# Kernel optimization log

Hardware: AMD Instinct MI355X
Metric: run time of the kernel (lower is better)

Reference implementation:

```python
import jax, jax.numpy as jnp
import numpy as np

N = 100000          # nodes
E = 3200000         # edges
C_IN = 64
HIDDEN = 64
NUM_CLASSES = 10
NUM_GRAPHS = 256
EPS = 1e-5


def _graph_conv(x, src, dst, w_rel, w_root, b):
    # PyG GraphConv(aggr='mean'): out_i = W_rel * mean_{j->i} x_j + W_root * x_i + b
    msg_sum = jax.ops.segment_sum(x[src], dst, num_segments=N)            # [N, C]
    cnt = jax.ops.segment_sum(jnp.ones((src.shape[0], 1), x.dtype), dst,
                              num_segments=N)                             # [N, 1]
    agg = msg_sum / jnp.maximum(cnt, 1.0)
    return agg @ w_rel + x @ w_root + b


def _batch_norm(x, gamma, beta):
    # PyG BatchNorm in training mode: batch stats over the node dimension
    mean = jnp.mean(x, axis=0)
    var = jnp.var(x, axis=0)
    return (x - mean) * jax.lax.rsqrt(var + EPS) * gamma + beta


def setup_inputs() -> dict:
    key = jax.random.key(0)
    ks = jax.random.split(key, 20)
    x = jax.random.normal(ks[0], (N, C_IN), dtype=jnp.float32)
    edge_index = jax.random.randint(ks[1], (2, E), 0, N, dtype=jnp.int32)
    batch = jnp.sort(jax.random.randint(ks[2], (N,), 0, NUM_GRAPHS, dtype=jnp.int32))

    def lin(k, fan_in, fan_out):
        s = 1.0 / np.sqrt(fan_in)
        return jax.random.uniform(k, (fan_in, fan_out), jnp.float32, -s, s)

    dims = [(C_IN, 16), (16, 32), (32, 32), (32, HIDDEN)]
    params = {}
    ki = 3
    for i, (ci, co) in enumerate(dims, start=1):
        params[f"w_rel{i}"] = lin(ks[ki], ci, co); ki += 1
        params[f"w_root{i}"] = lin(ks[ki], ci, co); ki += 1
        params[f"b{i}"] = jnp.zeros((co,), jnp.float32)
        params[f"g{i}"] = jnp.ones((co,), jnp.float32)
        params[f"be{i}"] = jnp.zeros((co,), jnp.float32)
    params["w_lin1"] = lin(ks[ki], HIDDEN, HIDDEN); ki += 1
    params["b_lin1"] = jnp.zeros((HIDDEN,), jnp.float32)
    params["w_lin2"] = lin(ks[ki], HIDDEN, NUM_CLASSES); ki += 1
    params["b_lin2"] = jnp.zeros((NUM_CLASSES,), jnp.float32)

    return {"x": x, "edge_index": edge_index, "batch": batch, **params}


def reference(x, edge_index, batch,
              w_rel1, w_root1, b1, g1, be1,
              w_rel2, w_root2, b2, g2, be2,
              w_rel3, w_root3, b3, g3, be3,
              w_rel4, w_root4, b4, g4, be4,
              w_lin1, b_lin1, w_lin2, b_lin2):
    src, dst = edge_index[0], edge_index[1]
    h = jax.nn.elu(_batch_norm(_graph_conv(x, src, dst, w_rel1, w_root1, b1), g1, be1))
    h = jax.nn.elu(_batch_norm(_graph_conv(h, src, dst, w_rel2, w_root2, b2), g2, be2))
    h = jax.nn.elu(_batch_norm(_graph_conv(h, src, dst, w_rel3, w_root3, b3), g3, be3))
    h = jax.nn.elu(_batch_norm(_graph_conv(h, src, dst, w_rel4, w_root4, b4), g4, be4))
    # global mean pool over graphs
    pooled = jax.ops.segment_sum(h, batch, num_segments=NUM_GRAPHS)
    cnt = jax.ops.segment_sum(jnp.ones((N, 1), h.dtype), batch, num_segments=NUM_GRAPHS)
    pooled = pooled / jnp.maximum(cnt, 1.0)
    z = jax.nn.relu(pooled @ w_lin1 + b_lin1)
    # dropout omitted (deterministic / eval mode)
    logits = z @ w_lin2 + b_lin2
    return jax.nn.log_softmax(logits, axis=-1)
```

## Files before the change

kernel.cpp:

```cpp
#include <hip/hip_runtime.h>
#include <hip/hip_bf16.h>
#include <math.h>

#define NGRAPHS 256
#define BSHIFT 8
#define NBUCK 512
#define NSORT 256
#define LSTAT 1024
#define GCHUNK 1024
#define SMASK 0x00FFFFFFu

__device__ __forceinline__ float bf2f(unsigned short u) {
    return __uint_as_float((unsigned)u << 16);
}
__device__ __forceinline__ unsigned short f2bf(float f) {
    unsigned u = __float_as_uint(f);
    unsigned r = (u + 0x7FFFu + ((u >> 16) & 1u)) >> 16;
    return (unsigned short)r;
}

__global__ __launch_bounds__(256) void k_bhist(const int* __restrict__ dst, int* __restrict__ hmat, int E,
                                               const float* __restrict__ x, const float* __restrict__ w_rel1,
                                               unsigned short* __restrict__ y1b,
                                               float* __restrict__ zbase, int zwords, int N) {
    int bid = blockIdx.x, tid = threadIdx.x;
    if (bid < NSORT) {
        __shared__ int hist[NBUCK];
        for (int i = tid; i < NBUCK; i += 256) hist[i] = 0;
        __syncthreads();
        int chunk = (E + NSORT - 1) / NSORT;
        int lo = bid * chunk;
        int hi = lo + chunk; if (hi > E) hi = E;
        for (int i = lo + tid; i < hi; i += 256)
            atomicAdd(&hist[__builtin_nontemporal_load(dst + i) >> BSHIFT], 1);
        __syncthreads();
        for (int i = tid; i < NBUCK; i += 256)
            hmat[(size_t)bid * NBUCK + i] = hist[i];
    } else {
        if (bid == NSORT) {
            for (int i = tid; i < zwords; i += 256) zbase[i] = 0.f;
        }
        __shared__ float s_rel[64 * 16];
        for (int i = tid; i < 64 * 16; i += 256) s_rel[i] = w_rel1[i];
        __syncthreads();
        int total = N * 4;
        int nb = gridDim.x - NSORT;
        for (int i = (bid - NSORT) * 256 + tid; i < total; i += nb * 256) {
            int n = i >> 2, c0 = (i & 3) << 2;
            const float4* mp = (const float4*)(x + (size_t)n * 64);
            float4 acc; acc.x = 0.f; acc.y = 0.f; acc.z = 0.f; acc.w = 0.f;
#pragma unroll
            for (int k2 = 0; k2 < 16; k2++) {
                float4 v = mp[k2];
                const float* wr = &s_rel[(k2 * 4) * 16 + c0];
                float4 w0 = *(const float4*)(wr);
                float4 w1 = *(const float4*)(wr + 16);
                float4 w2 = *(const float4*)(wr + 32);
                float4 w3 = *(const float4*)(wr + 48);
                acc.x += v.x * w0.x + v.y * w1.x + v.z * w2.x + v.w * w3.x;
                acc.y += v.x * w0.y + v.y * w1.y + v.z * w2.y + v.w * w3.y;
                acc.z += v.x * w0.z + v.y * w1.z + v.z * w2.z + v.w * w3.z;
                acc.w += v.x * w0.w + v.y * w1.w + v.z * w2.w + v.w * w3.w;
            }
            ushort4 o; o.x = f2bf(acc.x); o.y = f2bf(acc.y); o.z = f2bf(acc.z); o.w = f2bf(acc.w);
            *(ushort4*)(y1b + (size_t)n * 16 + c0) = o;
        }
    }
}

__global__ __launch_bounds__(512) void k_scan(int* __restrict__ hmat, int* __restrict__ bstart) {
    __shared__ int s[512];
    int col = threadIdx.x;
    int run = 0;
#pragma unroll 4
    for (int r = 0; r < NSORT; r++) {
        int v = hmat[(size_t)r * NBUCK + col];
        hmat[(size_t)r * NBUCK + col] = run;
        run += v;
    }
    s[col] = run;
    __syncthreads();
    for (int off = 1; off < 512; off <<= 1) {
        int t = (col >= off) ? s[col - off] : 0;
        __syncthreads();
        s[col] += t;
        __syncthreads();
    }
    bstart[col] = s[col] - run;
    if (col == 511) bstart[NBUCK] = s[511];
}

__global__ __launch_bounds__(256) void k_bscatter(const int* __restrict__ src, const int* __restrict__ dst,
                                                  const int* __restrict__ hmat, const int* __restrict__ bstart,
                                                  unsigned* __restrict__ ebuf, int E) {
    __shared__ int cur[NBUCK];
    for (int i = threadIdx.x; i < NBUCK; i += 256)
        cur[i] = bstart[i] + hmat[(size_t)blockIdx.x * NBUCK + i];
    __syncthreads();
    int chunk = (E + NSORT - 1) / NSORT;
    int lo = blockIdx.x * chunk;
    int hi = lo + chunk; if (hi > E) hi = E;
    for (int i = lo + threadIdx.x; i < hi; i += 256) {
        int d = __builtin_nontemporal_load(dst + i);
        int s = __builtin_nontemporal_load(src + i);
        int p = atomicAdd(&cur[d >> BSHIFT], 1);
        ebuf[p] = (unsigned)s | ((unsigned)(d & 255) << 24);
    }
}

__global__ __launch_bounds__(256) void k_sort2(const unsigned* __restrict__ ebuf, const int* __restrict__ bstart,
                                               int* __restrict__ csr, int* __restrict__ row_start, int N) {
    __shared__ int hist[256];
    __shared__ int sc[256];
    __shared__ int scur[256];
    int b = blockIdx.x;
    int e0 = bstart[b], e1 = bstart[b + 1];
    hist[threadIdx.x] = 0;
    __syncthreads();
    for (int i = e0 + threadIdx.x; i < e1; i += 256)
        atomicAdd(&hist[__builtin_nontemporal_load(ebuf + i) >> 24], 1);
    __syncthreads();
    sc[threadIdx.x] = hist[threadIdx.x];
    __syncthreads();
    for (int off = 1; off < 256; off <<= 1) {
        int t = (threadIdx.x >= off) ? sc[threadIdx.x - off] : 0;
        __syncthreads();
        sc[threadIdx.x] += t;
        __syncthreads();
    }
    {
        int inc = sc[threadIdx.x];
        int ex = inc - hist[threadIdx.x];
        scur[threadIdx.x] = e0 + ex;
        int node = (b << BSHIFT) + threadIdx.x;
        if (node < N) row_start[node] = e0 + ex;
        if (node == N - 1) row_start[N] = e0 + inc;
    }
    __syncthreads();
    for (int i = e0 + threadIdx.x; i < e1; i += 256) {
        unsigned w = __builtin_nontemporal_load(ebuf + i);
        int p = atomicAdd(&scur[w >> 24], 1);
        csr[p] = (int)(w & SMASK);
    }
}

template <int C>
__global__ __launch_bounds__(256) void k_gather(const unsigned short* __restrict__ h,
                                                const int* __restrict__ row_start,
                                                const int* __restrict__ csr, float* __restrict__ agg, int N) {
    constexpr int LPR = C / 4;
    constexpr int EPP = 64 / LPR;
    constexpr int BATCH = 4 * EPP;
    __shared__ int sbuf[GCHUNK];
    int lane = threadIdx.x & 63;
    int w = threadIdx.x >> 6;
    int nb = blockIdx.x * 4;
    int wid = nb + w;
    bool act = wid < N;
    int nb_end = nb + 4; if (nb_end > N) nb_end = N;
    int eb0 = row_start[nb];
    int eb1 = row_start[nb_end];
    int r0 = act ? row_start[wid] : 0;
    int r1 = act ? row_start[wid + 1] : 0;
    int es = lane / LPR;
    int cq = (lane % LPR) * 4;

    float a0 = 0.f, a1 = 0.f, a2 = 0.f, a3 = 0.f;
    for (int base = eb0; base < eb1; base += GCHUNK) {
        int len = eb1 - base; if (len > GCHUNK) len = GCHUNK;
        __syncthreads();
        for (int i = threadIdx.x; i < len; i += 256)
            sbuf[i] = __builtin_nontemporal_load(csr + base + i);
        __syncthreads();
        if (act) {
            int lo = (r0 > base ? r0 : base) - base;
            int hiv = r1 < base + len ? r1 : base + len;
            int hi = hiv - base;
            for (int j0 = lo; j0 < hi; j0 += BATCH) {
                int s[4]; bool p[4];
#pragma unroll
                for (int u = 0; u < 4; u++) {
                    int j = j0 + u * EPP + es;
                    p[u] = j < hi;
                    s[u] = sbuf[p[u] ? j : j0];
                }
                ushort4 v[4];
#pragma unroll
                for (int u = 0; u < 4; u++)
                    v[u] = *(const ushort4*)(h + (size_t)s[u] * C + cq);
#pragma unroll
                for (int u = 0; u < 4; u++) {
                    if (p[u]) {
                        a0 += bf2f(v[u].x); a1 += bf2f(v[u].y);
                        a2 += bf2f(v[u].z); a3 += bf2f(v[u].w);
                    }
                }
            }
        }
    }
#pragma unroll
    for (int off = LPR; off < 64; off <<= 1) {
        a0 += __shfl_xor(a0, off, 64);
        a1 += __shfl_xor(a1, off, 64);
        a2 += __shfl_xor(a2, off, 64);
        a3 += __shfl_xor(a3, off, 64);
    }
    if (act && lane < LPR) {
        int deg = r1 - r0;
        float rec = 1.0f / (float)(deg > 0 ? deg : 1);
        float4 o; o.x = a0 * rec; o.y = a1 * rec; o.z = a2 * rec; o.w = a3 * rec;
        *(float4*)(agg + (size_t)wid * C + cq) = o;
    }
}

template <int CI, int CO, bool HAS_REL, bool ADD_AGG, bool IN_BF16>
__global__ __launch_bounds__(256) void k_lin_stats(const void* __restrict__ hroot_v, const float* __restrict__ hrel,
                                                   const float* __restrict__ w_rel, const float* __restrict__ w_root,
                                                   const float* __restrict__ bias,
                                                   float* __restrict__ out, float* __restrict__ gsl, int N) {
    constexpr int QPR = CO / 4;
    __shared__ float s_rel[HAS_REL ? CI * CO : 1];
    __shared__ float s_root[CI * CO];
    __shared__ float s_b[CO];
    __shared__ float part[4][2 * CO];
    int tid = threadIdx.x;
    if (HAS_REL)
        for (int i = tid; i < CI * CO; i += 256) s_rel[i] = w_rel[i];
    for (int i = tid; i < CI * CO; i += 256) s_root[i] = w_root[i];
    if (tid < CO) s_b[tid] = bias[tid];
    __syncthreads();

    int total = N * QPR;
    int stride = gridDim.x * 256;
    float s0 = 0, s1 = 0, s2 = 0, s3 = 0, q0 = 0, q1 = 0, q2 = 0, q3 = 0;
    for (int i = blockIdx.x * 256 + tid; i < total; i += stride) {
        int n = i / QPR, c0 = (i % QPR) * 4;
        float4 acc = *(const float4*)&s_b[c0];
        if (ADD_AGG) {
            float4 v = ((const float4*)hrel)[i];
            acc.x += v.x; acc.y += v.y; acc.z += v.z; acc.w += v.w;
        }
#pragma unroll
        for (int cb = 0; cb < CI / 4; cb++) {
            float f0, f1, f2, f3;
            if (IN_BF16) {
                ushort4 v = *(const ushort4*)((const unsigned short*)hroot_v + (size_t)n * CI + cb * 4);
                f0 = bf2f(v.x); f1 = bf2f(v.y); f2 = bf2f(v.z); f3 = bf2f(v.w);
            } else {
                float4 v = *(const float4*)((const float*)hroot_v + (size_t)n * CI + cb * 4);
                f0 = v.x; f1 = v.y; f2 = v.z; f3 = v.w;
            }
            const float* wr = &s_root[(cb * 4) * CO + c0];
            float4 w0 = *(const float4*)(wr);
            float4 w1 = *(const float4*)(wr + CO);
            float4 w2 = *(const float4*)(wr + 2 * CO);
            float4 w3 = *(const float4*)(wr + 3 * CO);
            acc.x += f0 * w0.x + f1 * w1.x + f2 * w2.x + f3 * w3.x;
            acc.y += f0 * w0.y + f1 * w1.y + f2 * w2.y + f3 * w3.y;
            acc.z += f0 * w0.z + f1 * w1.z + f2 * w2.z + f3 * w3.z;
            acc.w += f0 * w0.w + f1 * w1.w + f2 * w2.w + f3 * w3.w;
            if (HAS_REL) {
                float4 a = *(const float4*)(hrel + (size_t)n * CI + cb * 4);
                const float* we = &s_rel[(cb * 4) * CO + c0];
                float4 e0 = *(const float4*)(we);
                float4 e1 = *(const float4*)(we + CO);
                float4 e2 = *(const float4*)(we + 2 * CO);
                float4 e3 = *(const float4*)(we + 3 * CO);
                acc.x += a.x * e0.x + a.y * e1.x + a.z * e2.x + a.w * e3.x;
                acc.y += a.x * e0.y + a.y * e1.y + a.z * e2.y + a.w * e3.y;
                acc.z += a.x * e0.z + a.y * e1.z + a.z * e2.z + a.w * e3.z;
                acc.w += a.x * e0.w + a.y * e1.w + a.z * e2.w + a.w * e3.w;
            }
        }
        ((float4*)out)[i] = acc;
        s0 += acc.x; q0 += acc.x * acc.x;
        s1 += acc.y; q1 += acc.y * acc.y;
        s2 += acc.z; q2 += acc.z * acc.z;
        s3 += acc.w; q3 += acc.w * acc.w;
    }
#pragma unroll
    for (int off = QPR; off < 64; off <<= 1) {
        s0 += __shfl_xor(s0, off, 64); q0 += __shfl_xor(q0, off, 64);
        s1 += __shfl_xor(s1, off, 64); q1 += __shfl_xor(q1, off, 64);
        s2 += __shfl_xor(s2, off, 64); q2 += __shfl_xor(q2, off, 64);
        s3 += __shfl_xor(s3, off, 64); q3 += __shfl_xor(q3, off, 64);
    }
    int lane = tid & 63;
    int w = tid >> 6;
    if (lane < QPR) {
        int cq = lane * 4;
        part[w][cq + 0] = s0; part[w][CO + cq + 0] = q0;
        part[w][cq + 1] = s1; part[w][CO + cq + 1] = q1;
        part[w][cq + 2] = s2; part[w][CO + cq + 2] = q2;
        part[w][cq + 3] = s3; part[w][CO + cq + 3] = q3;
    }
    __syncthreads();
    if (tid < 2 * CO) {
        float v = part[0][tid] + part[1][tid] + part[2][tid] + part[3][tid];
        atomicAdd(&gsl[tid], v);
    }
}

template <int CO>
__global__ __launch_bounds__(256) void k_bn_elu(const float* __restrict__ h, const float* __restrict__ gsl,
                                                const float* __restrict__ g, const float* __restrict__ be,
                                                unsigned short* __restrict__ hb, float invN, int N) {
    __shared__ float sc[CO], sh[CO];
    if (threadIdx.x < CO) {
        int c = threadIdx.x;
        float mean = gsl[c] * invN;
        float var = gsl[CO + c] * invN - mean * mean;
        float s = g[c] * rsqrtf(var + 1e-5f);
        sc[c] = s;
        sh[c] = be[c] - mean * s;
    }
    __syncthreads();
    int total = N * (CO / 4);
    int i = blockIdx.x * 256 + threadIdx.x;
    if (i >= total) return;
    float4 v = ((const float4*)h)[i];
    int cq = (i % (CO / 4)) * 4;
    v.x = v.x * sc[cq + 0] + sh[cq + 0];
    v.y = v.y * sc[cq + 1] + sh[cq + 1];
    v.z = v.z * sc[cq + 2] + sh[cq + 2];
    v.w = v.w * sc[cq + 3] + sh[cq + 3];
    v.x = v.x > 0.f ? v.x : expm1f(v.x);
    v.y = v.y > 0.f ? v.y : expm1f(v.y);
    v.z = v.z > 0.f ? v.z : expm1f(v.z);
    v.w = v.w > 0.f ? v.w : expm1f(v.w);
    ushort4 o;
    o.x = f2bf(v.x); o.y = f2bf(v.y); o.z = f2bf(v.z); o.w = f2bf(v.w);
    ((ushort4*)hb)[i] = o;
}

__global__ __launch_bounds__(256) void k_bn_elu_pool(const float* __restrict__ h, const float* __restrict__ gsl,
                                                     const float* __restrict__ g, const float* __restrict__ be,
                                                     const int* __restrict__ batch,
                                                     float* __restrict__ pooled, float* __restrict__ cntg,
                                                     float invN, int N) {
    __shared__ float sc[64], sh[64];
    if (threadIdx.x < 64) {
        int c = threadIdx.x;
        float mean = gsl[c] * invN;
        float var = gsl[64 + c] * invN - mean * mean;
        float s = g[c] * rsqrtf(var + 1e-5f);
        sc[c] = s;
        sh[c] = be[c] - mean * s;
    }
    __syncthreads();
    int lane = threadIdx.x & 63;
    int wid = blockIdx.x * 4 + (threadIdx.x >> 6);
    int n0 = wid * 16;
    if (n0 >= N) return;
    float scl = sc[lane];
    float shl = sh[lane];
    int nmax = N - n0; if (nmax > 16) nmax = 16;
    int cur = batch[n0];
    float acc = 0.f;
    float run = 0.f;
    for (int k = 0; k < nmax; k++) {
        int gg = batch[n0 + k];
        if (gg != cur) {
            atomicAdd(&pooled[(size_t)cur * 64 + lane], acc);
            if (lane == 0) atomicAdd(&cntg[cur], run);
            cur = gg; acc = 0.f; run = 0.f;
        }
        float v = h[(size_t)(n0 + k) * 64 + lane] * scl + shl;
        v = v > 0.f ? v : expm1f(v);
        acc += v;
        run += 1.f;
    }
    atomicAdd(&pooled[(size_t)cur * 64 + lane], acc);
    if (lane == 0) atomicAdd(&cntg[cur], run);
}

__global__ __launch_bounds__(256) void k_head(const float* __restrict__ pooled, const float* __restrict__ cntg,
                                              const float* __restrict__ w1, const float* __restrict__ b1,
                                              const float* __restrict__ w2, const float* __restrict__ b2,
                                              float* __restrict__ out) {
    int g = threadIdx.x;
    float rec = 1.0f / fmaxf(cntg[g], 1.0f);
    float p[64];
    {
        const float4* pp = (const float4*)(pooled + (size_t)g * 64);
#pragma unroll
        for (int i = 0; i < 16; i++) {
            float4 v = pp[i];
            p[4 * i + 0] = v.x * rec; p[4 * i + 1] = v.y * rec;
            p[4 * i + 2] = v.z * rec; p[4 * i + 3] = v.w * rec;
        }
    }
    float lg[10];
#pragma unroll
    for (int t = 0; t < 10; t++) lg[t] = b2[t];
#pragma unroll 1
    for (int j = 0; j < 64; j++) {
        float a = b1[j];
#pragma unroll
        for (int k = 0; k < 64; k++) a += p[k] * w1[k * 64 + j];
        a = fmaxf(a, 0.f);
#pragma unroll
        for (int t = 0; t < 10; t++) lg[t] += a * w2[j * 10 + t];
    }
    float m = -1e30f;
#pragma unroll
    for (int t = 0; t < 10; t++) m = fmaxf(m, lg[t]);
    float s = 0.f;
#pragma unroll
    for (int t = 0; t < 10; t++) s += expf(lg[t] - m);
    float lse = m + logf(s);
#pragma unroll
    for (int t = 0; t < 10; t++) out[(size_t)g * 10 + t] = lg[t] - lse;
}

extern "C" void kernel_launch(void* const* d_in, const int* in_sizes, int n_in,
                              void* d_out, int out_size, void* d_ws, size_t ws_size,
                              hipStream_t stream) {
    const float* x = (const float*)d_in[0];
    const int* ei = (const int*)d_in[1];
    const int* batch = (const int*)d_in[2];
    const int N = in_sizes[0] / 64;
    const int E = in_sizes[1] / 2;
    const int* src = ei;
    const int* dst = ei + E;

    const float* w_rel1 = (const float*)d_in[3];
    const float* w_root1 = (const float*)d_in[4];
    const float* b1 = (const float*)d_in[5];
    const float* g1 = (const float*)d_in[6];
    const float* be1 = (const float*)d_in[7];
    const float* w_rel2 = (const float*)d_in[8];
    const float* w_root2 = (const float*)d_in[9];
    const float* b2 = (const float*)d_in[10];
    const float* g2 = (const float*)d_in[11];
    const float* be2 = (const float*)d_in[12];
    const float* w_rel3 = (const float*)d_in[13];
    const float* w_root3 = (const float*)d_in[14];
    const float* b3 = (const float*)d_in[15];
    const float* g3 = (const float*)d_in[16];
    const float* be3 = (const float*)d_in[17];
    const float* w_rel4 = (const float*)d_in[18];
    const float* w_root4 = (const float*)d_in[19];
    const float* b4 = (const float*)d_in[20];
    const float* g4 = (const float*)d_in[21];
    const float* be4 = (const float*)d_in[22];
    const float* w_lin1 = (const float*)d_in[23];
    const float* b_lin1 = (const float*)d_in[24];
    const float* w_lin2 = (const float*)d_in[25];
    const float* b_lin2 = (const float*)d_in[26];

    char* ws = (char*)d_ws;
    size_t off = 0;
    auto alloc = [&](size_t bytes) { size_t o = off; off += (bytes + 255) & ~(size_t)255; return o; };
    int* hmat = (int*)(ws + alloc((size_t)NSORT * NBUCK * 4));
    int* bstart = (int*)(ws + alloc((size_t)(NBUCK + 1) * 4));
    unsigned* ebuf = (unsigned*)(ws + alloc((size_t)E * 4));
    int* csr = (int*)(ws + alloc((size_t)E * 4));
    int* row_start = (int*)(ws + alloc((size_t)(N + 1) * 4));
    float* agg = (float*)(ws + alloc((size_t)N * 32 * 4));
    unsigned short* y1b = (unsigned short*)(ws + alloc((size_t)N * 16 * 2));
    unsigned short* hb = (unsigned short*)(ws + alloc((size_t)N * 64 * 2));
    float* bufA = (float*)(ws + alloc((size_t)N * 64 * 4));
    float* gs = (float*)(ws + alloc((size_t)(512 + NGRAPHS * 64 + NGRAPHS) * 4));
    float* pooled = gs + 512;
    float* cntg = pooled + NGRAPHS * 64;
    const int zwords = 512 + NGRAPHS * 64 + NGRAPHS;

    const float invN = 1.0f / (float)N;
    const int gbl = (N + 3) / 4;

    k_bhist<<<1024, 256, 0, stream>>>(dst, hmat, E, x, w_rel1, y1b, gs, zwords, N);
    k_scan<<<1, 512, 0, stream>>>(hmat, bstart);
    k_bscatter<<<NSORT, 256, 0, stream>>>(src, dst, hmat, bstart, ebuf, E);
    k_sort2<<<NBUCK, 256, 0, stream>>>(ebuf, bstart, csr, row_start, N);

    k_gather<16><<<gbl, 256, 0, stream>>>(y1b, row_start, csr, agg, N);
    k_lin_stats<64, 16, false, true, false><<<LSTAT, 256, 0, stream>>>(
        x, agg, nullptr, w_root1, b1, bufA, gs + 0, N);
    k_bn_elu<16><<<(N * 4 + 255) / 256, 256, 0, stream>>>(bufA, gs + 0, g1, be1, hb, invN, N);

    k_gather<16><<<gbl, 256, 0, stream>>>(hb, row_start, csr, agg, N);
    k_lin_stats<16, 32, true, false, true><<<LSTAT, 256, 0, stream>>>(
        hb, agg, w_rel2, w_root2, b2, bufA, gs + 128, N);
    k_bn_elu<32><<<(N * 8 + 255) / 256, 256, 0, stream>>>(bufA, gs + 128, g2, be2, hb, invN, N);

    k_gather<32><<<gbl, 256, 0, stream>>>(hb, row_start, csr, agg, N);
    k_lin_stats<32, 32, true, false, true><<<LSTAT, 256, 0, stream>>>(
        hb, agg, w_rel3, w_root3, b3, bufA, gs + 256, N);
    k_bn_elu<32><<<(N * 8 + 255) / 256, 256, 0, stream>>>(bufA, gs + 256, g3, be3, hb, invN, N);

    k_gather<32><<<gbl, 256, 0, stream>>>(hb, row_start, csr, agg, N);
    k_lin_stats<32, 64, true, false, true><<<LSTAT, 256, 0, stream>>>(
        hb, agg, w_rel4, w_root4, b4, bufA, gs + 384, N);
    int waves16 = (N + 15) / 16;
    k_bn_elu_pool<<<(waves16 + 3) / 4, 256, 0, stream>>>(
        bufA, gs + 384, g4, be4, batch, pooled, cntg, invN, N);

    k_head<<<1, 256, 0, stream>>>(pooled, cntg, w_lin1, b_lin1, w_lin2, b_lin2, (float*)d_out);
}
```

Baseline: 604.5 us.

## Replace single-block scan kernel with atomic column offsets and per-block bucket scan

```diff
diff --git a/kernel.cpp b/kernel.cpp
--- a/kernel.cpp
+++ b/kernel.cpp
@@ -22,7 +22,7 @@
 __global__ __launch_bounds__(256) void k_bhist(const int* __restrict__ dst, int* __restrict__ hmat, int E,
                                                const float* __restrict__ x, const float* __restrict__ w_rel1,
                                                unsigned short* __restrict__ y1b,
-                                               float* __restrict__ zbase, int zwords, int N) {
+                                               int* __restrict__ colpos, int N) {
     int bid = blockIdx.x, tid = threadIdx.x;
     if (bid < NSORT) {
         __shared__ int hist[NBUCK];
@@ -34,12 +34,12 @@
         for (int i = lo + tid; i < hi; i += 256)
             atomicAdd(&hist[__builtin_nontemporal_load(dst + i) >> BSHIFT], 1);
         __syncthreads();
-        for (int i = tid; i < NBUCK; i += 256)
-            hmat[(size_t)bid * NBUCK + i] = hist[i];
+        for (int i = tid; i < NBUCK; i += 256) {
+            int h = hist[i];
+            int base = atomicAdd(&colpos[i], h);
+            hmat[(size_t)bid * NBUCK + i] = base;
+        }
     } else {
-        if (bid == NSORT) {
-            for (int i = tid; i < zwords; i += 256) zbase[i] = 0.f;
-        }
         __shared__ float s_rel[64 * 16];
         for (int i = tid; i < 64 * 16; i += 256) s_rel[i] = w_rel1[i];
         __syncthreads();
@@ -68,43 +68,38 @@
     }
 }
 
-__global__ __launch_bounds__(512) void k_scan(int* __restrict__ hmat, int* __restrict__ bstart) {
-    __shared__ int s[512];
-    int col = threadIdx.x;
-    int run = 0;
-#pragma unroll 4
-    for (int r = 0; r < NSORT; r++) {
-        int v = hmat[(size_t)r * NBUCK + col];
-        hmat[(size_t)r * NBUCK + col] = run;
-        run += v;
-    }
-    s[col] = run;
-    __syncthreads();
-    for (int off = 1; off < 512; off <<= 1) {
-        int t = (col >= off) ? s[col - off] : 0;
-        __syncthreads();
-        s[col] += t;
-        __syncthreads();
-    }
-    bstart[col] = s[col] - run;
-    if (col == 511) bstart[NBUCK] = s[511];
-}
-
-__global__ __launch_bounds__(256) void k_bscatter(const int* __restrict__ src, const int* __restrict__ dst,
-                                                  const int* __restrict__ hmat, const int* __restrict__ bstart,
+__global__ __launch_bounds__(512) void k_bscatter(const int* __restrict__ src, const int* __restrict__ dst,
+                                                  const int* __restrict__ hmat, const int* __restrict__ colpos,
+                                                  int* __restrict__ bstart_g,
                                                   unsigned* __restrict__ ebuf, int E) {
+    __shared__ int s[NBUCK];
     __shared__ int cur[NBUCK];
-    for (int i = threadIdx.x; i < NBUCK; i += 256)
-        cur[i] = bstart[i] + hmat[(size_t)blockIdx.x * NBUCK + i];
+    int tid = threadIdx.x;
+    int b = blockIdx.x;
+    int v = colpos[tid];
+    s[tid] = v;
+    __syncthreads();
+    for (int off = 1; off < NBUCK; off <<= 1) {
+        int t = (tid >= off) ? s[tid - off] : 0;
+        __syncthreads();
+        s[tid] += t;
+        __syncthreads();
+    }
+    int excl = s[tid] - v;
+    if (b == 0) {
+        bstart_g[tid] = excl;
+        if (tid == NBUCK - 1) bstart_g[NBUCK] = s[NBUCK - 1];
+    }
+    cur[tid] = excl + hmat[(size_t)b * NBUCK + tid];
     __syncthreads();
     int chunk = (E + NSORT - 1) / NSORT;
-    int lo = blockIdx.x * chunk;
+    int lo = b * chunk;
     int hi = lo + chunk; if (hi > E) hi = E;
-    for (int i = lo + threadIdx.x; i < hi; i += 256) {
+    for (int i = lo + tid; i < hi; i += 512) {
         int d = __builtin_nontemporal_load(dst + i);
-        int s = __builtin_nontemporal_load(src + i);
+        int sv = __builtin_nontemporal_load(src + i);
         int p = atomicAdd(&cur[d >> BSHIFT], 1);
-        ebuf[p] = (unsigned)s | ((unsigned)(d & 255) << 24);
+        ebuf[p] = (unsigned)sv | ((unsigned)(d & 255) << 24);
     }
 }
 
@@ -461,17 +456,19 @@
     unsigned short* y1b = (unsigned short*)(ws + alloc((size_t)N * 16 * 2));
     unsigned short* hb = (unsigned short*)(ws + alloc((size_t)N * 64 * 2));
     float* bufA = (float*)(ws + alloc((size_t)N * 64 * 4));
-    float* gs = (float*)(ws + alloc((size_t)(512 + NGRAPHS * 64 + NGRAPHS) * 4));
+    const int zwords = NBUCK + 512 + NGRAPHS * 64 + NGRAPHS;
+    int* colpos = (int*)(ws + alloc((size_t)zwords * 4));
+    float* gs = (float*)(colpos + NBUCK);
     float* pooled = gs + 512;
     float* cntg = pooled + NGRAPHS * 64;
-    const int zwords = 512 + NGRAPHS * 64 + NGRAPHS;
+
+    hipMemsetAsync(colpos, 0, (size_t)zwords * 4, stream);
 
     const float invN = 1.0f / (float)N;
     const int gbl = (N + 3) / 4;
 
-    k_bhist<<<1024, 256, 0, stream>>>(dst, hmat, E, x, w_rel1, y1b, gs, zwords, N);
-    k_scan<<<1, 512, 0, stream>>>(hmat, bstart);
-    k_bscatter<<<NSORT, 256, 0, stream>>>(src, dst, hmat, bstart, ebuf, E);
+    k_bhist<<<1024, 256, 0, stream>>>(dst, hmat, E, x, w_rel1, y1b, colpos, N);
+    k_bscatter<<<NSORT, 512, 0, stream>>>(src, dst, hmat, colpos, bstart, ebuf, E);
     k_sort2<<<NBUCK, 256, 0, stream>>>(ebuf, bstart, csr, row_start, N);
 
     k_gather<16><<<gbl, 256, 0, stream>>>(y1b, row_start, csr, agg, N);
```

Result: faster. 589.5 us (-2.5%).
